# Optimization experiments

Measured on AMD Instinct MI355X. Metric: run time of the kernel, lower is better.

## Reference

```python
import jax, jax.numpy as jnp
import numpy as np

CONTEXT = 256   # context_size
INITIAL = 32    # initial_size
HIDDEN = 256    # hidden_size
WINDOW = 64 - 1 # module stores window_size - 1
TEMP = 50000.0  # soft-argmax temperature
MAX_STEPS = CONTEXT - INITIAL  # cur_pt >= 1 guarantees >=1 index advance per step
B = 4096


def setup_inputs() -> dict:
    key = jax.random.key(0)
    ks = jax.random.split(key, 4)
    def lin_w(k, fan_in, fan_out):
        bound = 1.0 / np.sqrt(fan_in)
        return jax.random.uniform(k, (fan_in, fan_out), jnp.float32, -bound, bound)
    return {
        "x": jax.random.normal(ks[0], (B, CONTEXT), jnp.float32),
        "hid_W": lin_w(ks[1], HIDDEN, HIDDEN),
        "hid_b": jnp.zeros((HIDDEN,), jnp.float32),
        "in_W": lin_w(ks[2], INITIAL, HIDDEN),
        "in_b": jnp.zeros((HIDDEN,), jnp.float32),
        "pred_W": lin_w(ks[3], HIDDEN, WINDOW),
        "pred_b": jnp.zeros((WINDOW,), jnp.float32),
    }


def reference(x, hid_W, hid_b, in_W, in_b, pred_W, pred_b):
    # with per-item active masks. Padded/dense outputs:
    #   pts  [B, MAX_STEPS] : predicted change points (last point dropped, rest zero-padded)
    #   mx   [B, CONTEXT]   : all sigmoid-masked slices scattered back to their positions
    # returned concatenated as [B, MAX_STEPS + CONTEXT].
    Bv = x.shape[0]
    rows = jnp.arange(Bv)[:, None]
    jW = jnp.arange(WINDOW, dtype=jnp.float32)
    iI = jnp.arange(INITIAL)
    iWin = jnp.arange(WINDOW)

    def step(carry, _):
        last, hidden, masked_x, count = carry
        active = last < CONTEXT                       # torch: skip items whose last pt >= context
        last_long = last.astype(jnp.int32)            # floor (last >= INITIAL > 0)
        # slice x[i, last-INITIAL : last]; first step last=INITIAL -> x[:, 0:INITIAL]
        idx = last_long[:, None] - INITIAL + iI       # [B, I]
        slices = jnp.take_along_axis(x, idx, axis=1)
        new_hidden = jnp.tanh(hidden @ hid_W + hid_b + slices @ in_W + in_b)
        hidden = jnp.where(active[:, None], new_hidden, hidden)
        w = new_hidden @ pred_W + pred_b              # [B, WINDOW]
        p = jax.nn.softmax(w * TEMP, axis=-1)
        cur_pt = jnp.minimum(p @ jW + 1.0, float(WINDOW))        # soft-argmax + 1, clamped
        seq_end = jnp.minimum(cur_pt + last, float(CONTEXT))
        seq_end_long = seq_end.astype(jnp.int32)
        # masked slice: mask = 1 - sigmoid(j - cur_pt), j in [0, seq_end_long - last_long)
        pos = last_long[:, None] + iWin                            # [B, WINDOW]
        valid = (pos < seq_end_long[:, None]) & active[:, None]
        mask = 1.0 - jax.nn.sigmoid(jW[None, :] - cur_pt[:, None])
        pos_c = jnp.clip(pos, 0, CONTEXT - 1)
        xg = jnp.take_along_axis(x, pos_c, axis=1)
        contrib = jnp.where(valid, mask * xg, 0.0)
        masked_x = masked_x.at[rows, pos_c].add(contrib)           # segments are disjoint
        last = jnp.where(active, seq_end, last)
        count = count + active.astype(jnp.int32)
        return (last, hidden, masked_x, count), jnp.where(active, seq_end, 0.0)

    init = (jnp.full((Bv,), float(INITIAL), jnp.float32),
            jnp.ones((Bv, HIDDEN), jnp.float32),
            jnp.zeros_like(x),
            jnp.zeros((Bv,), jnp.int32))
    (last, hidden, masked_x, count), ys = jax.lax.scan(step, init, None, length=MAX_STEPS)
    pts = ys.T                                                    # [B, MAX_STEPS]
    keep = jnp.arange(MAX_STEPS)[None, :] < (count - 1)[:, None]  # torch drops last pt per item
    pts = jnp.where(keep, pts, 0.0)
    return jnp.concatenate([pts, masked_x], axis=1)               # [B, MAX_STEPS + CONTEXT]
```

## Files before the change

### kernel.cpp

```cpp
#include <hip/hip_runtime.h>
#include <math.h>


#define CTX     256
#define INIT    32
#define HID     256
#define WIN     63
#define MSTEPS  224
#define OUTROW  (MSTEPS + CTX)
#define IT      4
#define NT      512
#define KSPLIT  112

__global__ void __launch_bounds__(NT)
cpp_kernel(const float* __restrict__ x,
           const float* __restrict__ hid_W,
           const float* __restrict__ hid_b,
           const float* __restrict__ in_W,
           const float* __restrict__ in_b,
           const float* __restrict__ pred_W,
           const float* __restrict__ pred_b,
           float* __restrict__ out)
{
    __shared__ double s_x[IT][CTX];
    __shared__ double s_hid[IT][HID];
    __shared__ double s_scr[IT][8][64];
    __shared__ float  s_last[IT];
    __shared__ int    s_lastl[IT];
    __shared__ int    s_act[IT];

    const int tid   = threadIdx.x;
    const int lane  = tid & 63;
    const int q     = tid >> 6;
    const int j     = tid & (HID - 1);
    const int half  = tid >> 8;
    const int item0 = blockIdx.x * IT;

    for (int idx = tid; idx < IT * CTX; idx += NT)
        s_x[idx >> 8][idx & 255] = (double)x[(size_t)(item0 + (idx >> 8)) * CTX + (idx & 255)];
    for (int idx = tid; idx < IT * HID; idx += NT)
        s_hid[idx >> 8][idx & 255] = 1.0;
    for (int idx = tid; idx < IT * OUTROW; idx += NT)
        out[(size_t)item0 * OUTROW + idx] = 0.0f;
    if (tid < IT) { s_last[tid] = (float)INIT; s_lastl[tid] = INIT; s_act[tid] = 1; }

    const double bias = (half == 0) ? ((double)hid_b[j] + (double)in_b[j]) : 0.0;
    double* const red = &s_scr[0][0][0];

    __syncthreads();

    int sc = 0;

    for (int iter = 0; iter < MSTEPS; ++iter) {
        int lastl[IT], act[IT];
        #pragma unroll
        for (int it = 0; it < IT; ++it) { lastl[it] = s_lastl[it]; act[it] = s_act[it]; }
        if (!(act[0] | act[1] | act[2] | act[3])) break;

        double acc[IT];
        #pragma unroll
        for (int it = 0; it < IT; ++it) acc[it] = bias;

        if (half == 0) {
            int sb[IT];
            #pragma unroll
            for (int it = 0; it < IT; ++it) sb[it] = lastl[it] - INIT;
            #pragma unroll 4
            for (int m = 0; m < INIT; ++m) {
                const double wv = (double)in_W[m * HID + j];
                #pragma unroll
                for (int it = 0; it < IT; ++it)
                    acc[it] = fma(s_x[it][sb[it] + m], wv, acc[it]);
            }
        }

        {
            const int kbeg = (half == 0) ? 0 : KSPLIT;
            const int kend = (half == 0) ? KSPLIT : HID;
            for (int k = kbeg; k < kend; k += 4) {
                double2 hA[IT], hB[IT];
                #pragma unroll
                for (int it = 0; it < IT; ++it) {
                    hA[it] = *(const double2*)&s_hid[it][k];
                    hB[it] = *(const double2*)&s_hid[it][k + 2];
                }
                const double w0 = (double)hid_W[(size_t)(k + 0) * HID + j];
                const double w1 = (double)hid_W[(size_t)(k + 1) * HID + j];
                const double w2 = (double)hid_W[(size_t)(k + 2) * HID + j];
                const double w3 = (double)hid_W[(size_t)(k + 3) * HID + j];
                #pragma unroll
                for (int it = 0; it < IT; ++it) {
                    acc[it] = fma(hA[it].x, w0, acc[it]);
                    acc[it] = fma(hA[it].y, w1, acc[it]);
                    acc[it] = fma(hB[it].x, w2, acc[it]);
                    acc[it] = fma(hB[it].y, w3, acc[it]);
                }
            }
        }

        if (half == 1) {
            #pragma unroll
            for (int it = 0; it < IT; ++it) red[it * HID + j] = acc[it];
        }
        __syncthreads();

        if (half == 0) {
            float nh[IT];
            #pragma unroll
            for (int it = 0; it < IT; ++it) {
                acc[it] += red[it * HID + j];
                nh[it] = tanhf((float)acc[it]);
            }
            #pragma unroll
            for (int it = 0; it < IT; ++it)
                if (act[it]) s_hid[it][j] = (double)nh[it];
        }
        __syncthreads();

        double pacc[IT] = {0.0, 0.0, 0.0, 0.0};
        if (lane < WIN) {
            const int kb = q * 32;
            #pragma unroll 4
            for (int kk = 0; kk < 32; ++kk) {
                const int k = kb + kk;
                const double wv = (double)pred_W[k * WIN + lane];
                #pragma unroll
                for (int it = 0; it < IT; ++it)
                    pacc[it] = fma(s_hid[it][k], wv, pacc[it]);
            }
        }
        #pragma unroll
        for (int it = 0; it < IT; ++it) s_scr[it][q][lane] = pacc[it];
        __syncthreads();

        if (q < IT) {
            const int it = q;
            float t = -INFINITY;
            if (lane < WIN) {
                const double wv = s_scr[it][0][lane] + s_scr[it][1][lane]
                                + s_scr[it][2][lane] + s_scr[it][3][lane]
                                + s_scr[it][4][lane] + s_scr[it][5][lane]
                                + s_scr[it][6][lane] + s_scr[it][7][lane]
                                + (double)pred_b[lane];
                t = (float)wv * 50000.0f;
            }
            float mx = t;
            #pragma unroll
            for (int off = 32; off > 0; off >>= 1)
                mx = fmaxf(mx, __shfl_xor(mx, off));
            const float e = (lane < WIN) ? expf(t - mx) : 0.0f;
            float S = e;
            #pragma unroll
            for (int off = 32; off > 0; off >>= 1)
                S += __shfl_xor(S, off);
            const float p = e / S;
            float D = p * (float)lane;
            #pragma unroll
            for (int off = 32; off > 0; off >>= 1)
                D += __shfl_xor(D, off);
            float cur = D + 1.0f;
            cur = fminf(cur, 63.0f);
            float se = cur + s_last[it];
            se = fminf(se, 256.0f);
            const int sel = (int)se;

            if (act[it]) {
                float* orow = out + (size_t)(item0 + it) * OUTROW;
                if (lane < WIN) {
                    const int pos = lastl[it] + lane;
                    if (pos < sel) {
                        const float msk = 1.0f / (1.0f + expf((float)lane - cur));
                        orow[MSTEPS + pos] = msk * (float)s_x[it][pos];
                    }
                }
                if (lane == 0) {
                    if (se < 256.0f) orow[sc] = se;
                    s_last[it]  = se;
                    s_lastl[it] = sel;
                    s_act[it]   = (se < 256.0f) ? 1 : 0;
                }
                sc++;
            }
        }
        __syncthreads();
    }
}

extern "C" void kernel_launch(void* const* d_in, const int* in_sizes, int n_in,
                              void* d_out, int out_size, void* d_ws, size_t ws_size,
                              hipStream_t stream) {
    const float* x      = (const float*)d_in[0];
    const float* hid_W  = (const float*)d_in[1];
    const float* hid_b  = (const float*)d_in[2];
    const float* in_W   = (const float*)d_in[3];
    const float* in_b   = (const float*)d_in[4];
    const float* pred_W = (const float*)d_in[5];
    const float* pred_b = (const float*)d_in[6];
    float* out = (float*)d_out;

    const int B = in_sizes[0] / CTX;
    const int nblocks = B / IT;
    cpp_kernel<<<nblocks, NT, 0, stream>>>(x, hid_W, hid_b, in_W, in_b,
                                           pred_W, pred_b, out);
}
```

Before: 328.9 us.

## Use persistent blocks with atomic work-stealing to refill finished item slots

Launches a fixed grid of 512 persistent blocks. Whenever an item in one of a block's four slots finishes its ragged scan, that slot takes a new item index from a global atomic counter and reloads its x slice and hidden state. This is meant to stop a block from idling until its slowest item is done. In exchange it adds an extra counter-init kernel launch, per-refill global atomics and loads, and fewer resident blocks overall.

Measured after the change: 318.6 us. 3.1% less time.

```diff
diff --git a/kernel.cpp b/kernel.cpp
--- a/kernel.cpp
+++ b/kernel.cpp
@@ -11,6 +11,10 @@
 #define IT      4
 #define NT      512
 #define KSPLIT  112
+#define NBLK    512
+#define NSLOT   (NBLK * IT)
+
+__global__ void init_counter_kernel(int* cnt, int v) { *cnt = v; }
 
 __global__ void __launch_bounds__(NT)
 cpp_kernel(const float* __restrict__ x,
@@ -20,38 +24,47 @@
            const float* __restrict__ in_b,
            const float* __restrict__ pred_W,
            const float* __restrict__ pred_b,
-           float* __restrict__ out)
+           float* __restrict__ out,
+           int* __restrict__ cnt, int B)
 {
     __shared__ double s_x[IT][CTX];
     __shared__ double s_hid[IT][HID];
     __shared__ double s_scr[IT][8][64];
-    __shared__ float  s_last[IT];
     __shared__ int    s_lastl[IT];
     __shared__ int    s_act[IT];
 
-    const int tid   = threadIdx.x;
-    const int lane  = tid & 63;
-    const int q     = tid >> 6;
-    const int j     = tid & (HID - 1);
-    const int half  = tid >> 8;
-    const int item0 = blockIdx.x * IT;
-
-    for (int idx = tid; idx < IT * CTX; idx += NT)
-        s_x[idx >> 8][idx & 255] = (double)x[(size_t)(item0 + (idx >> 8)) * CTX + (idx & 255)];
-    for (int idx = tid; idx < IT * HID; idx += NT)
-        s_hid[idx >> 8][idx & 255] = 1.0;
-    for (int idx = tid; idx < IT * OUTROW; idx += NT)
-        out[(size_t)item0 * OUTROW + idx] = 0.0f;
-    if (tid < IT) { s_last[tid] = (float)INIT; s_lastl[tid] = INIT; s_act[tid] = 1; }
+    const int tid  = threadIdx.x;
+    const int lane = tid & 63;
+    const int q    = tid >> 6;
+    const int j    = tid & (HID - 1);
+    const int half = tid >> 8;
 
     const double bias = (half == 0) ? ((double)hid_b[j] + (double)in_b[j]) : 0.0;
     double* const red = &s_scr[0][0][0];
 
+    int   myitem = -1;
+    float mylast = (float)INIT;
+    int   sc = 0;
+
+    if (q < IT) {
+        const int item = blockIdx.x * IT + q;
+        if (item < B) {
+            myitem = item;
+            float* orow = out + (size_t)item * OUTROW;
+            for (int idx = lane; idx < OUTROW; idx += 64) orow[idx] = 0.0f;
+            const float4 xv = *(const float4*)&x[(size_t)item * CTX + lane * 4];
+            s_x[q][lane * 4 + 0] = (double)xv.x;
+            s_x[q][lane * 4 + 1] = (double)xv.y;
+            s_x[q][lane * 4 + 2] = (double)xv.z;
+            s_x[q][lane * 4 + 3] = (double)xv.w;
+            #pragma unroll
+            for (int u = 0; u < 4; ++u) s_hid[q][lane + 64 * u] = 1.0;
+            if (lane == 0) { s_lastl[q] = INIT; s_act[q] = 1; }
+        } else if (lane == 0) { s_lastl[q] = INIT; s_act[q] = 0; }
+    }
     __syncthreads();
 
-    int sc = 0;
-
-    for (int iter = 0; iter < MSTEPS; ++iter) {
+    for (int iter = 0; iter < (1 << 18); ++iter) {
         int lastl[IT], act[IT];
         #pragma unroll
         for (int it = 0; it < IT; ++it) { lastl[it] = s_lastl[it]; act[it] = s_act[it]; }
@@ -64,7 +77,10 @@
         if (half == 0) {
             int sb[IT];
             #pragma unroll
-            for (int it = 0; it < IT; ++it) sb[it] = lastl[it] - INIT;
+            for (int it = 0; it < IT; ++it) {
+                int l = lastl[it]; if (l > CTX) l = CTX;
+                sb[it] = l - INIT;
+            }
             #pragma unroll 4
             for (int m = 0; m < INIT; ++m) {
                 const double wv = (double)in_W[m * HID + j];
@@ -73,7 +89,6 @@
                     acc[it] = fma(s_x[it][sb[it] + m], wv, acc[it]);
             }
         }
-
         {
             const int kbeg = (half == 0) ? 0 : KSPLIT;
             const int kend = (half == 0) ? KSPLIT : HID;
@@ -105,15 +120,11 @@
         __syncthreads();
 
         if (half == 0) {
-            float nh[IT];
             #pragma unroll
             for (int it = 0; it < IT; ++it) {
                 acc[it] += red[it * HID + j];
-                nh[it] = tanhf((float)acc[it]);
-            }
-            #pragma unroll
-            for (int it = 0; it < IT; ++it)
-                if (act[it]) s_hid[it][j] = (double)nh[it];
+                if (act[it]) s_hid[it][j] = (double)tanhf((float)acc[it]);
+            }
         }
         __syncthreads();
 
@@ -133,7 +144,7 @@
         for (int it = 0; it < IT; ++it) s_scr[it][q][lane] = pacc[it];
         __syncthreads();
 
-        if (q < IT) {
+        if (q < IT && act[q]) {
             const int it = q;
             float t = -INFINITY;
             if (lane < WIN) {
@@ -158,28 +169,42 @@
             #pragma unroll
             for (int off = 32; off > 0; off >>= 1)
                 D += __shfl_xor(D, off);
-            float cur = D + 1.0f;
-            cur = fminf(cur, 63.0f);
-            float se = cur + s_last[it];
-            se = fminf(se, 256.0f);
+            float cur = fminf(D + 1.0f, 63.0f);
+            float se = fminf(cur + mylast, 256.0f);
             const int sel = (int)se;
 
-            if (act[it]) {
-                float* orow = out + (size_t)(item0 + it) * OUTROW;
-                if (lane < WIN) {
-                    const int pos = lastl[it] + lane;
-                    if (pos < sel) {
-                        const float msk = 1.0f / (1.0f + expf((float)lane - cur));
-                        orow[MSTEPS + pos] = msk * (float)s_x[it][pos];
-                    }
-                }
-                if (lane == 0) {
-                    if (se < 256.0f) orow[sc] = se;
-                    s_last[it]  = se;
-                    s_lastl[it] = sel;
-                    s_act[it]   = (se < 256.0f) ? 1 : 0;
-                }
-                sc++;
+            float* orow = out + (size_t)myitem * OUTROW;
+            if (lane < WIN) {
+                const int pos = lastl[it] + lane;
+                if (pos < sel) {
+                    const float msk = 1.0f / (1.0f + expf((float)lane - cur));
+                    orow[MSTEPS + pos] = msk * (float)s_x[it][pos];
+                }
+            }
+            const bool done = (se >= 256.0f);
+            if (lane == 0 && !done) { orow[sc] = se; s_lastl[it] = sel; }
+            sc++;
+            mylast = se;
+
+            if (done) {
+                int nid = 0;
+                if (lane == 0) nid = atomicAdd(cnt, 1);
+                nid = __shfl(nid, 0);
+                if (nid < B) {
+                    myitem = nid; mylast = (float)INIT; sc = 0;
+                    float* nrow = out + (size_t)nid * OUTROW;
+                    for (int idx = lane; idx < OUTROW; idx += 64) nrow[idx] = 0.0f;
+                    const float4 xv = *(const float4*)&x[(size_t)nid * CTX + lane * 4];
+                    s_x[it][lane * 4 + 0] = (double)xv.x;
+                    s_x[it][lane * 4 + 1] = (double)xv.y;
+                    s_x[it][lane * 4 + 2] = (double)xv.z;
+                    s_x[it][lane * 4 + 3] = (double)xv.w;
+                    #pragma unroll
+                    for (int u = 0; u < 4; ++u) s_hid[it][lane + 64 * u] = 1.0;
+                    if (lane == 0) s_lastl[it] = INIT;
+                } else {
+                    if (lane == 0) s_act[it] = 0;
+                }
             }
         }
         __syncthreads();
@@ -197,9 +222,10 @@
     const float* pred_W = (const float*)d_in[5];
     const float* pred_b = (const float*)d_in[6];
     float* out = (float*)d_out;
+    int*   cnt = (int*)d_ws;
 
     const int B = in_sizes[0] / CTX;
-    const int nblocks = B / IT;
-    cpp_kernel<<<nblocks, NT, 0, stream>>>(x, hid_W, hid_b, in_W, in_b,
-                                           pred_W, pred_b, out);
+    init_counter_kernel<<<1, 1, 0, stream>>>(cnt, NSLOT);
+    cpp_kernel<<<NBLK, NT, 0, stream>>>(x, hid_W, hid_b, in_W, in_b,
+                                        pred_W, pred_b, out, cnt, B);
 }
```
